# Optimization experiments

Measured on AMD Instinct MI355X. Metric: run time of the kernel, lower is better.

## Reference

```python
import jax, jax.numpy as jnp
import numpy as np

BETA = 0.02
TOPK = 5  # torch.topk(A, k=5) is hard-coded; forward arg k is ignored


def setup_inputs() -> dict:
    key = jax.random.key(0)
    k1, k2, k3 = jax.random.split(key, 3)
    B, Cx, C1, CA, N, D, L = 4, 16, 16, 8, 1024, 64, 64
    x = jax.random.normal(k1, (B, Cx, N, D), dtype=jnp.float32)
    A = jax.random.normal(k2, (B, CA, N, N), dtype=jnp.float32)
    mask = jax.random.uniform(k3, (B, C1, N, L), dtype=jnp.float32)
    return {"x": x, "A": A, "mask": mask, "k": 5}


def reference(x, A, mask, k):
    # x: (B,Cx,N,D), A: (B,CA,N,N), mask: (B,C1,N,L)
    # S = softmax(x @ x^T) over last dim, then mean over channel dim -> (B,1,N,N)
    S = jax.nn.softmax(jnp.einsum('bcnd,bcmd->bcnm', x, x), axis=-1)
    S = jnp.mean(S, axis=1, keepdims=True)
    # mask similarity: (B,C1,N,N)
    mm = jnp.einsum('bcnl,bcml->bcnm', mask, mask)
    mask_weight = jax.nn.sigmoid(S * mm / jnp.sqrt(jnp.float32(10.0)))
    # A averaged over its channel dim, broadcast-added -> (B,C1,N,N)
    A_out = jnp.mean(A, axis=1, keepdims=True) + BETA * mask_weight
    # top-5 neighbors per row, gather their mask rows, reduce with max
    _, idx = jax.lax.top_k(A_out, TOPK)              # (B,C1,N,5) int32
    # mask_select[b,c,i,j,l] = mask[b,c,idx[b,c,i,j],l]
    gather = jax.vmap(jax.vmap(lambda m, i: m[i]))(mask, idx)  # (B,C1,N,5,L)
    mask_updated = jnp.max(gather, axis=-2)          # (B,C1,N,L)
    return A_out, mask_updated
```

## Files before the change

### kernel.cpp

```cpp
#include <hip/hip_runtime.h>
#include <math.h>

#define NB 4
#define NCX 16
#define NC1 16
#define NCA 8
#define NN 1024
#define ND 64
#define NL 64
#define LSTRIDE 1028

typedef __attribute__((ext_vector_type(8))) short bf16x8;
typedef __attribute__((ext_vector_type(4))) float f32x4;
typedef unsigned short u16;
typedef unsigned int u32;

__device__ __forceinline__ u16 f2b(float f) {
    u32 u = __float_as_uint(f);
    return (u16)((u + 0x7FFFu + ((u >> 16) & 1u)) >> 16);
}

__device__ __forceinline__ bf16x8 cvt8(const float* __restrict__ p) {
    float4 a = *(const float4*)p;
    float4 b = *(const float4*)(p + 4);
    bf16x8 r;
    r[0] = (short)f2b(a.x); r[1] = (short)f2b(a.y);
    r[2] = (short)f2b(a.z); r[3] = (short)f2b(a.w);
    r[4] = (short)f2b(b.x); r[5] = (short)f2b(b.y);
    r[6] = (short)f2b(b.z); r[7] = (short)f2b(b.w);
    return r;
}

__device__ __forceinline__ float sigm(float z) {
    return 1.0f / (1.0f + __expf(-z));
}

__global__ __launch_bounds__(256) void k_prep(const float* __restrict__ x,
                                              u16* __restrict__ xb) {
    int id = blockIdx.x * 256 + threadIdx.x;
    const float4* x4 = (const float4*)x;
    float4 a = x4[2 * id];
    float4 b = x4[2 * id + 1];
    union { u16 u[8]; uint4 v; } o;
    o.u[0] = f2b(a.x); o.u[1] = f2b(a.y); o.u[2] = f2b(a.z); o.u[3] = f2b(a.w);
    o.u[4] = f2b(b.x); o.u[5] = f2b(b.y); o.u[6] = f2b(b.z); o.u[7] = f2b(b.w);
    ((uint4*)xb)[id] = o.v;
}

__global__ __launch_bounds__(256) void k_meanA(const float* __restrict__ A,
                                               float* __restrict__ meanA) {
    int id = blockIdx.x * 256 + threadIdx.x;
    int b  = id >> 18;
    int e  = id & 262143;
    const float4* A4 = (const float4*)A;
    float4 s = A4[(size_t)(b * NCA) * 262144 + e];
#pragma unroll
    for (int c = 1; c < NCA; ++c) {
        float4 v = A4[(size_t)(b * NCA + c) * 262144 + e];
        s.x += v.x; s.y += v.y; s.z += v.z; s.w += v.w;
    }
    s.x *= 0.125f; s.y *= 0.125f; s.z *= 0.125f; s.w *= 0.125f;
    ((float4*)meanA)[id] = s;
}

__global__ __launch_bounds__(1024, 4) void k_smean3(const u16* __restrict__ xb,
                                                    float* __restrict__ Smean) {
    __shared__ float L[16 * LSTRIDE];
    const int t  = threadIdx.x;
    const int w  = t >> 6;
    const int l  = t & 63;
    const int lm = l & 15;
    const int lq = l >> 4;
    const int i0 = blockIdx.x * 16;
    const int b  = blockIdx.y;
    const int rb = lq * 4;

    float mean[16];
#pragma unroll
    for (int u = 0; u < 16; ++u) mean[u] = 0.f;

    const int arow = i0 + lm;

    for (int c = 0; c < NCX; ++c) {
        const u16* Xc = xb + (size_t)(b * NCX + c) * NN * ND;
        bf16x8 a0 = *(const bf16x8*)(Xc + arow * ND + lq * 8);
        bf16x8 a1 = *(const bf16x8*)(Xc + arow * ND + 32 + lq * 8);
#pragma unroll
        for (int tt = 0; tt < 4; ++tt) {
            int j0 = w * 64 + tt * 16;
            const u16* Bp = Xc + (j0 + lm) * ND;
            bf16x8 b0 = *(const bf16x8*)(Bp + lq * 8);
            bf16x8 b1 = *(const bf16x8*)(Bp + 32 + lq * 8);
            f32x4 acc = {0.f, 0.f, 0.f, 0.f};
            acc = __builtin_amdgcn_mfma_f32_16x16x32_bf16(a0, b0, acc, 0, 0, 0);
            acc = __builtin_amdgcn_mfma_f32_16x16x32_bf16(a1, b1, acc, 0, 0, 0);
            int col = j0 + lm;
            L[(rb + 0) * LSTRIDE + col] = acc[0];
            L[(rb + 1) * LSTRIDE + col] = acc[1];
            L[(rb + 2) * LSTRIDE + col] = acc[2];
            L[(rb + 3) * LSTRIDE + col] = acc[3];
        }
        __syncthreads();
        {
            const float* Lp = &L[w * LSTRIDE];
            float v[16];
#pragma unroll
            for (int u = 0; u < 4; ++u) {
                float4 q = *(const float4*)&Lp[4 * l + 256 * u];
                v[4 * u + 0] = q.x; v[4 * u + 1] = q.y;
                v[4 * u + 2] = q.z; v[4 * u + 3] = q.w;
            }
            float m = v[0];
#pragma unroll
            for (int u = 1; u < 16; ++u) m = fmaxf(m, v[u]);
#pragma unroll
            for (int off = 32; off; off >>= 1) m = fmaxf(m, __shfl_xor(m, off, 64));
            float sum = 0.f;
#pragma unroll
            for (int u = 0; u < 16; ++u) { v[u] = __expf(v[u] - m); sum += v[u]; }
#pragma unroll
            for (int off = 32; off; off >>= 1) sum += __shfl_xor(sum, off, 64);
            float r = 1.0f / sum;
#pragma unroll
            for (int u = 0; u < 16; ++u) mean[u] = fmaf(v[u], r, mean[u]);
        }
        __syncthreads();
    }
    float* Sp = Smean + ((size_t)b * NN + (i0 + w)) * NN;
#pragma unroll
    for (int u = 0; u < 4; ++u) {
        float4 o;
        o.x = mean[4 * u + 0] * 0.0625f;
        o.y = mean[4 * u + 1] * 0.0625f;
        o.z = mean[4 * u + 2] * 0.0625f;
        o.w = mean[4 * u + 3] * 0.0625f;
        *(float4*)(Sp + 4 * l + 256 * u) = o;
    }
}

__global__ __launch_bounds__(1024, 4) void k_final3(const float* __restrict__ mask,
                                                    const float* __restrict__ Smean,
                                                    const float* __restrict__ meanA,
                                                    float* __restrict__ Aout,
                                                    float* __restrict__ maskUpd) {
    __shared__ float L[16 * LSTRIDE];
    const int t  = threadIdx.x;
    const int w  = t >> 6;
    const int l  = t & 63;
    const int lm = l & 15;
    const int lq = l >> 4;
    const int i0 = blockIdx.x * 16;
    const int c1 = blockIdx.y;
    const int b  = blockIdx.z;
    const int rb = lq * 4;

    const float* mbase = mask + (size_t)(b * NC1 + c1) * NN * NL;

    bf16x8 a0 = cvt8(mbase + (i0 + lm) * NL + lq * 8);
    bf16x8 a1 = cvt8(mbase + (i0 + lm) * NL + 32 + lq * 8);
#pragma unroll
    for (int tt = 0; tt < 4; ++tt) {
        int j0 = w * 64 + tt * 16;
        const float* Bp = mbase + (j0 + lm) * NL;
        bf16x8 b0 = cvt8(Bp + lq * 8);
        bf16x8 b1 = cvt8(Bp + 32 + lq * 8);
        f32x4 acc = {0.f, 0.f, 0.f, 0.f};
        acc = __builtin_amdgcn_mfma_f32_16x16x32_bf16(a0, b0, acc, 0, 0, 0);
        acc = __builtin_amdgcn_mfma_f32_16x16x32_bf16(a1, b1, acc, 0, 0, 0);
        int col = j0 + lm;
        L[(rb + 0) * LSTRIDE + col] = acc[0];
        L[(rb + 1) * LSTRIDE + col] = acc[1];
        L[(rb + 2) * LSTRIDE + col] = acc[2];
        L[(rb + 3) * LSTRIDE + col] = acc[3];
    }
    __syncthreads();

    const int row = i0 + w;
    const float* Lp = &L[w * LSTRIDE];
    const float* Sp = Smean + ((size_t)b * NN + row) * NN;
    const float* Mp = meanA + ((size_t)b * NN + row) * NN;
    float* Ap = Aout + ((size_t)(b * NC1 + c1) * NN + row) * NN;

    float lg[16];
#pragma unroll
    for (int u = 0; u < 4; ++u) {
        int j = 4 * l + 256 * u;
        float4 mm4 = *(const float4*)&Lp[j];
        float4 S4  = *(const float4*)(Sp + j);
        float4 M4  = *(const float4*)(Mp + j);
        float4 o;
        o.x = M4.x + 0.02f * sigm(S4.x * mm4.x * 0.31622776601683794f);
        o.y = M4.y + 0.02f * sigm(S4.y * mm4.y * 0.31622776601683794f);
        o.z = M4.z + 0.02f * sigm(S4.z * mm4.z * 0.31622776601683794f);
        o.w = M4.w + 0.02f * sigm(S4.w * mm4.w * 0.31622776601683794f);
        *(float4*)(Ap + j) = o;
        lg[4 * u + 0] = o.x; lg[4 * u + 1] = o.y;
        lg[4 * u + 2] = o.z; lg[4 * u + 3] = o.w;
    }

    int idxs[5];
#pragma unroll
    for (int p = 0; p < 5; ++p) {
        float bv = lg[0];
        int   bj = 4 * l;
#pragma unroll
        for (int k = 1; k < 16; ++k) {
            int j = 4 * l + 256 * (k >> 2) + (k & 3);
            if (lg[k] > bv) { bv = lg[k]; bj = j; }
        }
#pragma unroll
        for (int off = 32; off; off >>= 1) {
            float ov = __shfl_xor(bv, off, 64);
            int   oj = __shfl_xor(bj, off, 64);
            if (ov > bv || (ov == bv && oj < bj)) { bv = ov; bj = oj; }
        }
        idxs[p] = bj;
        const bool mine = ((bj & 255) >> 2) == l;
        const int  ck   = (bj >> 8) * 4 + (bj & 3);
#pragma unroll
        for (int k = 0; k < 16; ++k)
            lg[k] = (mine && k == ck) ? -INFINITY : lg[k];
    }
    float mx = mbase[(size_t)idxs[0] * NL + l];
#pragma unroll
    for (int p = 1; p < 5; ++p)
        mx = fmaxf(mx, mbase[(size_t)idxs[p] * NL + l]);
    maskUpd[((size_t)(b * NC1 + c1) * NN + row) * NL + l] = mx;
}

extern "C" void kernel_launch(void* const* d_in, const int* in_sizes, int n_in,
                              void* d_out, int out_size, void* d_ws, size_t ws_size,
                              hipStream_t stream) {
    const float* x    = (const float*)d_in[0];
    const float* A    = (const float*)d_in[1];
    const float* mask = (const float*)d_in[2];
    float* out     = (float*)d_out;
    float* Aout    = out;
    float* maskUpd = out + (size_t)NB * NC1 * NN * NN;
    float* meanA   = (float*)d_ws;
    float* Smean   = meanA + (size_t)NB * NN * NN;
    u16*   xb      = (u16*)Aout;

    hipLaunchKernelGGL(k_prep, dim3((NB * NCX * NN * ND / 8) / 256), dim3(256), 0,
                       stream, x, xb);
    hipLaunchKernelGGL(k_meanA, dim3((NB * NN * NN / 4) / 256), dim3(256), 0, stream,
                       A, meanA);
    hipLaunchKernelGGL(k_smean3, dim3(NN / 16, NB), dim3(1024), 0, stream,
                       xb, Smean);
    hipLaunchKernelGGL(k_final3, dim3(NN / 16, NC1, NB), dim3(1024), 0, stream,
                       mask, Smean, meanA, Aout, maskUpd);
}
```

Baseline: 693.8 us.

## Split softmax-mean over channel groups, pre-convert mask to bf16, prefetch S

The channel loop of the softmax-mean kernel is split into four channel groups across a third grid dimension, raising the block count from 256 to 1024. Each group writes partial sums into the unused output buffer, and a new reduction kernel adds them. When the workspace is large enough, the mask is converted to bf16 once up front, so the final kernel loads bf16 instead of converting fp32 in every block. The final kernel also loads its Smean row before the barrier. The cost is an extra 16M-float partial write and read plus two more launches, and launch bounds now request 8 blocks per SM, which the 64KB of LDS per block may not allow.

```diff
diff --git a/kernel.cpp b/kernel.cpp
--- a/kernel.cpp
+++ b/kernel.cpp
@@ -9,6 +9,7 @@
 #define ND 64
 #define NL 64
 #define LSTRIDE 1028
+#define NCG 4
 
 typedef __attribute__((ext_vector_type(8))) short bf16x8;
 typedef __attribute__((ext_vector_type(4))) float f32x4;
@@ -35,16 +36,16 @@
     return 1.0f / (1.0f + __expf(-z));
 }
 
-__global__ __launch_bounds__(256) void k_prep(const float* __restrict__ x,
-                                              u16* __restrict__ xb) {
+__global__ __launch_bounds__(256) void k_cvt(const float* __restrict__ src,
+                                             u16* __restrict__ dst) {
     int id = blockIdx.x * 256 + threadIdx.x;
-    const float4* x4 = (const float4*)x;
+    const float4* x4 = (const float4*)src;
     float4 a = x4[2 * id];
     float4 b = x4[2 * id + 1];
     union { u16 u[8]; uint4 v; } o;
     o.u[0] = f2b(a.x); o.u[1] = f2b(a.y); o.u[2] = f2b(a.z); o.u[3] = f2b(a.w);
     o.u[4] = f2b(b.x); o.u[5] = f2b(b.y); o.u[6] = f2b(b.z); o.u[7] = f2b(b.w);
-    ((uint4*)xb)[id] = o.v;
+    ((uint4*)dst)[id] = o.v;
 }
 
 __global__ __launch_bounds__(256) void k_meanA(const float* __restrict__ A,
@@ -63,8 +64,8 @@
     ((float4*)meanA)[id] = s;
 }
 
-__global__ __launch_bounds__(1024, 4) void k_smean3(const u16* __restrict__ xb,
-                                                    float* __restrict__ Smean) {
+__global__ __launch_bounds__(1024, 8) void k_smean4(const u16* __restrict__ xb,
+                                                    float* __restrict__ Spart) {
     __shared__ float L[16 * LSTRIDE];
     const int t  = threadIdx.x;
     const int w  = t >> 6;
@@ -73,6 +74,7 @@
     const int lq = l >> 4;
     const int i0 = blockIdx.x * 16;
     const int b  = blockIdx.y;
+    const int cg = blockIdx.z;
     const int rb = lq * 4;
 
     float mean[16];
@@ -81,7 +83,7 @@
 
     const int arow = i0 + lm;
 
-    for (int c = 0; c < NCX; ++c) {
+    for (int c = cg * 4; c < cg * 4 + 4; ++c) {
         const u16* Xc = xb + (size_t)(b * NCX + c) * NN * ND;
         bf16x8 a0 = *(const bf16x8*)(Xc + arow * ND + lq * 8);
         bf16x8 a1 = *(const bf16x8*)(Xc + arow * ND + 32 + lq * 8);
@@ -126,19 +128,35 @@
         }
         __syncthreads();
     }
-    float* Sp = Smean + ((size_t)b * NN + (i0 + w)) * NN;
+    float* Sp = Spart + (((size_t)(cg * NB + b)) * NN + (i0 + w)) * NN;
 #pragma unroll
     for (int u = 0; u < 4; ++u) {
         float4 o;
-        o.x = mean[4 * u + 0] * 0.0625f;
-        o.y = mean[4 * u + 1] * 0.0625f;
-        o.z = mean[4 * u + 2] * 0.0625f;
-        o.w = mean[4 * u + 3] * 0.0625f;
+        o.x = mean[4 * u + 0]; o.y = mean[4 * u + 1];
+        o.z = mean[4 * u + 2]; o.w = mean[4 * u + 3];
         *(float4*)(Sp + 4 * l + 256 * u) = o;
     }
 }
 
-__global__ __launch_bounds__(1024, 4) void k_final3(const float* __restrict__ mask,
+__global__ __launch_bounds__(256) void k_sred(const float* __restrict__ Spart,
+                                              float* __restrict__ Smean) {
+    int id = blockIdx.x * 256 + threadIdx.x;
+    int b  = id >> 18;
+    int e  = id & 262143;
+    const float4* P4 = (const float4*)Spart;
+    float4 s = P4[(size_t)b * 262144 + e];
+#pragma unroll
+    for (int g = 1; g < NCG; ++g) {
+        float4 v = P4[(size_t)(g * NB + b) * 262144 + e];
+        s.x += v.x; s.y += v.y; s.z += v.z; s.w += v.w;
+    }
+    s.x *= 0.0625f; s.y *= 0.0625f; s.z *= 0.0625f; s.w *= 0.0625f;
+    ((float4*)Smean)[id] = s;
+}
+
+template <bool MB>
+__global__ __launch_bounds__(1024, 8) void k_final4(const float* __restrict__ mask,
+                                                    const u16* __restrict__ maskb,
                                                     const float* __restrict__ Smean,
                                                     const float* __restrict__ meanA,
                                                     float* __restrict__ Aout,
@@ -153,17 +171,32 @@
     const int c1 = blockIdx.y;
     const int b  = blockIdx.z;
     const int rb = lq * 4;
+    const int row = i0 + w;
 
     const float* mbase = mask + (size_t)(b * NC1 + c1) * NN * NL;
-
-    bf16x8 a0 = cvt8(mbase + (i0 + lm) * NL + lq * 8);
-    bf16x8 a1 = cvt8(mbase + (i0 + lm) * NL + 32 + lq * 8);
+    const u16*   mbb   = maskb + (size_t)(b * NC1 + c1) * NN * NL;
+
+    bf16x8 a0, a1;
+    if (MB) {
+        a0 = *(const bf16x8*)(mbb + (i0 + lm) * NL + lq * 8);
+        a1 = *(const bf16x8*)(mbb + (i0 + lm) * NL + 32 + lq * 8);
+    } else {
+        a0 = cvt8(mbase + (i0 + lm) * NL + lq * 8);
+        a1 = cvt8(mbase + (i0 + lm) * NL + 32 + lq * 8);
+    }
 #pragma unroll
     for (int tt = 0; tt < 4; ++tt) {
         int j0 = w * 64 + tt * 16;
-        const float* Bp = mbase + (j0 + lm) * NL;
-        bf16x8 b0 = cvt8(Bp + lq * 8);
-        bf16x8 b1 = cvt8(Bp + 32 + lq * 8);
+        bf16x8 b0, b1;
+        if (MB) {
+            const u16* Bp = mbb + (j0 + lm) * NL;
+            b0 = *(const bf16x8*)(Bp + lq * 8);
+            b1 = *(const bf16x8*)(Bp + 32 + lq * 8);
+        } else {
+            const float* Bp = mbase + (j0 + lm) * NL;
+            b0 = cvt8(Bp + lq * 8);
+            b1 = cvt8(Bp + 32 + lq * 8);
+        }
         f32x4 acc = {0.f, 0.f, 0.f, 0.f};
         acc = __builtin_amdgcn_mfma_f32_16x16x32_bf16(a0, b0, acc, 0, 0, 0);
         acc = __builtin_amdgcn_mfma_f32_16x16x32_bf16(a1, b1, acc, 0, 0, 0);
@@ -173,11 +206,15 @@
         L[(rb + 2) * LSTRIDE + col] = acc[2];
         L[(rb + 3) * LSTRIDE + col] = acc[3];
     }
+
+    const float* Sp = Smean + ((size_t)b * NN + row) * NN;
+    float4 S4r[4];
+#pragma unroll
+    for (int u = 0; u < 4; ++u) S4r[u] = *(const float4*)(Sp + 4 * l + 256 * u);
+
     __syncthreads();
 
-    const int row = i0 + w;
     const float* Lp = &L[w * LSTRIDE];
-    const float* Sp = Smean + ((size_t)b * NN + row) * NN;
     const float* Mp = meanA + ((size_t)b * NN + row) * NN;
     float* Ap = Aout + ((size_t)(b * NC1 + c1) * NN + row) * NN;
 
@@ -186,7 +223,7 @@
     for (int u = 0; u < 4; ++u) {
         int j = 4 * l + 256 * u;
         float4 mm4 = *(const float4*)&Lp[j];
-        float4 S4  = *(const float4*)(Sp + j);
+        float4 S4  = S4r[u];
         float4 M4  = *(const float4*)(Mp + j);
         float4 o;
         o.x = M4.x + 0.02f * sigm(S4.x * mm4.x * 0.31622776601683794f);
@@ -239,14 +276,27 @@
     float* maskUpd = out + (size_t)NB * NC1 * NN * NN;
     float* meanA   = (float*)d_ws;
     float* Smean   = meanA + (size_t)NB * NN * NN;
-    u16*   xb      = (u16*)Aout;
-
-    hipLaunchKernelGGL(k_prep, dim3((NB * NCX * NN * ND / 8) / 256), dim3(256), 0,
+    u16*   maskb   = (u16*)(Smean + (size_t)NB * NN * NN);
+    const bool useMB = ws_size >= (size_t)(2 * NB * NN * NN * 4 + NB * NC1 * NN * NL * 2);
+
+    u16*   xb    = (u16*)Aout;
+    float* Spart = Aout + (size_t)16777216;
+
+    hipLaunchKernelGGL(k_cvt, dim3((NB * NCX * NN * ND / 8) / 256), dim3(256), 0,
                        stream, x, xb);
+    if (useMB)
+        hipLaunchKernelGGL(k_cvt, dim3((NB * NC1 * NN * NL / 8) / 256), dim3(256), 0,
+                           stream, mask, (u16*)maskb);
     hipLaunchKernelGGL(k_meanA, dim3((NB * NN * NN / 4) / 256), dim3(256), 0, stream,
                        A, meanA);
-    hipLaunchKernelGGL(k_smean3, dim3(NN / 16, NB), dim3(1024), 0, stream,
-                       xb, Smean);
-    hipLaunchKernelGGL(k_final3, dim3(NN / 16, NC1, NB), dim3(1024), 0, stream,
-                       mask, Smean, meanA, Aout, maskUpd);
-}
+    hipLaunchKernelGGL(k_smean4, dim3(NN / 16, NB, NCG), dim3(1024), 0, stream,
+                       xb, Spart);
+    hipLaunchKernelGGL(k_sred, dim3((NB * NN * NN / 4) / 256), dim3(256), 0, stream,
+                       Spart, Smean);
+    if (useMB)
+        hipLaunchKernelGGL(k_final4<true>, dim3(NN / 16, NC1, NB), dim3(1024), 0,
+                           stream, mask, maskb, Smean, meanA, Aout, maskUpd);
+    else
+        hipLaunchKernelGGL(k_final4<false>, dim3(NN / 16, NC1, NB), dim3(1024), 0,
+                           stream, mask, maskb, Smean, meanA, Aout, maskUpd);
+}
```

Result: faster. 593.4 us (-14.5%).
